# Performance work log

Measured on AMD Instinct MI355X. Metric: run time of the kernel, lower is better.

Reference implementation:

```python
import jax, jax.numpy as jnp
import numpy as np

SR = 22050
L = 2097153            # output_size = int(SR*95.109); equals NFFT//2+1 so spectral broadcast is well-defined
NFFT = 4194304         # 2**ceil(log2(L))
BANDS = [(1.0, 4.0), (4.0, 8.0), (8.0, 13.0), (13.0, 30.0), (30.0, 100.0), (100.0, 200.0)]
SPEC = [7.83, 528.0, 396.0, 2.5, 14.1, 432.0, 6.0, 30.0]
WIN = 15               # min(15, NFFT//100)
FREQS_NP = np.fft.rfftfreq(NFFT, 1.0 / SR).astype(np.float32)
FREQS = jnp.asarray(FREQS_NP)


def _freq_mod(sig, band_w, freq_w, harm_prog, tm_w1, tm_b1, tm_w2, tm_b2, tm_w3, tm_b3):
    t = jnp.arange(L, dtype=jnp.float32)
    Xf = jnp.fft.rfft(jnp.pad(sig, (0, NFFT - L)))            # [L] complex64
    # sequential band enhancements == product of per-band multipliers
    mult = jnp.ones((L,), jnp.float32)
    for b, (lo, hi) in enumerate(BANDS):
        c = (lo + hi) / 2.0
        w = (hi - lo) / 2.0
        mask = jnp.exp(-0.5 * ((FREQS - c) / (w / 2.0)) ** 2)
        mask = jnp.where((FREQS < lo) | (FREQS > hi), 0.0, mask)
        tmod = jnp.sin(2.0 * np.pi * c * t / SR)
        mult = mult * (1.0 + mask * band_w[b] * (1.0 + 0.2 * tmod))
    # harmonic progression (identical for every specific frequency -> compute once)
    tn = (t / L)[:, None]
    h = jax.nn.relu(tn @ tm_w1 + tm_b1)
    h = jax.nn.relu(h @ tm_w2 + tm_b2)
    mp = h @ tm_w3 + tm_b3                                    # [L, 8]
    chord_idx = jnp.floor(t / L * 8.0).astype(jnp.int32) % 8
    chord = harm_prog[chord_idx] * (1.0 + mp[:, 1] * jnp.sin(2.0 * np.pi * t / L))[:, None]
    prog_mean = chord.mean()
    # specific-frequency harmonic windows (static indices; commutative multiplies)
    smult = jnp.ones((L,), jnp.float32)
    for k, f in enumerate(SPEC):
        for m in (1.0, 2.0, 3.0, 4.0, 5.0):
            hf = f * m
            if hf >= SR / 2:
                continue
            hidx = int(np.argmin(np.abs(FREQS_NP - hf)))
            s = max(0, hidx - WIN)
            e = min(L - 1, hidx + WIN)
            win = jnp.asarray(np.exp(-0.5 * ((np.arange(s, e + 1) - hidx) / (WIN / 3.0)) ** 2).astype(np.float32))
            enh = freq_w[k] * win * (1.0 / m ** 1.2) * (1.0 + prog_mean)
            smult = smult.at[s:e + 1].multiply(1.0 + enh)
    Xf = Xf * mult * smult
    mag = jnp.abs(Xf)
    ph = jnp.angle(Xf)
    mag_s = jnp.concatenate([mag[:1], mag[1:-1] * 0.7 + mag[:-2] * 0.15 + mag[2:] * 0.15, mag[-1:]])
    Xc = mag_s * jnp.exp(1j * ph)
    return jnp.fft.irfft(Xc, n=NFFT)[:L]


def _conv1d(x, w, b, stride):
    y = jax.lax.conv_general_dilated(x, w, (stride,), [(2, 2)], dimension_numbers=("NCH", "OIH", "NCH"))
    return y + b[None, :, None]


def setup_inputs() -> dict:
    key = jax.random.key(0)
    ks = jax.random.split(key, 16)
    n = lambda k, s, sc=1.0: jax.random.normal(k, s, dtype=jnp.float32) * sc
    return {
        "z": n(ks[0], (1, 1, L)),
        "condition": n(ks[1], (1, 8)),
        "band_w": jnp.full((6,), 0.5, jnp.float32),
        "freq_w": jnp.full((8,), 0.3, jnp.float32),
        "harm_prog": n(ks[2], (8, 4)),
        "tm_w1": n(ks[3], (1, 32), 0.5), "tm_b1": jnp.zeros((32,), jnp.float32),
        "tm_w2": n(ks[4], (32, 16), 0.2), "tm_b2": jnp.zeros((16,), jnp.float32),
        "tm_w3": n(ks[5], (16, 8), 0.2), "tm_b3": jnp.zeros((8,), jnp.float32),
        "c1_w": n(ks[6], (32, 1, 5), 0.3), "c1_b": jnp.zeros((32,), jnp.float32),
        "c2_w": n(ks[7], (64, 32, 5), 0.08), "c2_b": jnp.zeros((64,), jnp.float32),
        "c3_w": n(ks[8], (128, 64, 5), 0.05), "c3_b": jnp.zeros((128,), jnp.float32),
        "mx_w1": n(ks[9], (192, 256), 0.07), "mx_b1": jnp.zeros((256,), jnp.float32),
        "mx_w2": n(ks[10], (256, 1), 0.06), "mx_b2": jnp.zeros((1,), jnp.float32),
    }


def reference(z, condition, band_w, freq_w, harm_prog, tm_w1, tm_b1, tm_w2, tm_b2, tm_w3, tm_b3,
              c1_w, c1_b, c2_w, c2_b, c3_w, c3_b, mx_w1, mx_b1, mx_w2, mx_b2):
    base = _freq_mod(z[0, 0], band_w, freq_w, harm_prog, tm_w1, tm_b1, tm_w2, tm_b2, tm_w3, tm_b3)[None, None, :]
    h = jax.nn.leaky_relu(_conv1d(base, c1_w, c1_b, 2), 0.2)
    h = jax.nn.leaky_relu(_conv1d(h, c2_w, c2_b, 2), 0.2)
    h = jax.nn.leaky_relu(_conv1d(h, c3_w, c3_b, 2), 0.2)
    feat = h.mean(axis=2)                                     # [1, 128]
    emb = jnp.zeros((1, 64), jnp.float32)                     # instrument_idx=None path
    mixed = jnp.concatenate([feat, emb], axis=1)              # [1, 192]
    out = jax.nn.leaky_relu(mixed @ mx_w1 + mx_b1, 0.2) @ mx_w2 + mx_b2
    return out
```

## Files before the change

kernel.cpp:

```cpp
#include <hip/hip_runtime.h>
#include <cmath>

#define LSIG  2097153
#define MH    2097152
#define NFFTC 4194304
#define NT    262144
#define NT64  32768
#define O1C   1048577
#define O2C   524289
#define O3C   262145

#define TO3   62
#define NB3   4229

#define A_OFF    0
#define B_OFF    16777216
#define PM_OFF   58720268
#define FEAT_OFF 58720272
#define W2Q_OFF  50331664
#define W3Q_OFF  50352144
#define W1Q_OFF  50434064

struct SmultTab { int hidx[40]; float inv12[40]; int fk[40]; int maxe; };

typedef short short8 __attribute__((ext_vector_type(8)));
typedef float f32x4v __attribute__((ext_vector_type(4)));

union AFrag { uint4 q; short8 s; };
union BFrag { uint4 q; unsigned int u[4]; short8 s; };

__device__ __forceinline__ float lrelu(float a){ return a > 0.0f ? a : 0.2f*a; }

__device__ __forceinline__ float hsin(float rev){ return __builtin_amdgcn_sinf(rev); }
__device__ __forceinline__ float hcos(float rev){ return __builtin_amdgcn_cosf(rev); }

__device__ __forceinline__ unsigned int rbf(float f) {
  unsigned int u = __float_as_uint(f);
  u += 0x7fffu + ((u >> 16) & 1u);
  return u >> 16;
}
__device__ __forceinline__ unsigned int pack_bf2(float a, float b) {
  return rbf(a) | (rbf(b) << 16);
}

__device__ __forceinline__ int swz1(int pos, int dw) {
  return (pos*16 + dw) ^ (((pos >> 1) & 7) << 2);
}
__device__ __forceinline__ int swz2(int pos, int dw) {
  return (pos*32 + dw) ^ (((pos >> 1) & 7) << 2);
}

__device__ __forceinline__ float2 cadd(float2 a, float2 b){ return make_float2(a.x+b.x, a.y+b.y); }
__device__ __forceinline__ float2 csub(float2 a, float2 b){ return make_float2(a.x-b.x, a.y-b.y); }
__device__ __forceinline__ float2 cmul(float2 a, float2 b){ return make_float2(a.x*b.x - a.y*b.y, a.x*b.y + a.y*b.x); }

template<bool FWD> __device__ __forceinline__ float2 jrot(float2 z){
  return FWD ? make_float2(z.y, -z.x) : make_float2(-z.y, z.x);
}

template<bool FWD> __device__ __forceinline__ void dft8(float2 v[8]) {
  const float cq = 0.70710678118654752440f;
  const float S  = FWD ? -1.0f : 1.0f;
  float2 e0 = cadd(v[0], v[4]), e1 = csub(v[0], v[4]);
  float2 e2 = cadd(v[2], v[6]), e3 = csub(v[2], v[6]);
  float2 E0 = cadd(e0, e2), E2 = csub(e0, e2);
  float2 jt = jrot<FWD>(e3);
  float2 E1 = cadd(e1, jt), E3 = csub(e1, jt);
  float2 o0 = cadd(v[1], v[5]), o1 = csub(v[1], v[5]);
  float2 o2 = cadd(v[3], v[7]), o3 = csub(v[3], v[7]);
  float2 O0 = cadd(o0, o2), O2 = csub(o0, o2);
  float2 jo = jrot<FWD>(o3);
  float2 O1 = cadd(o1, jo), O3 = csub(o1, jo);
  float2 T1 = make_float2(cq, S*cq), T3 = make_float2(-cq, S*cq);
  float2 w1 = cmul(T1, O1);
  float2 w2 = jrot<FWD>(O2);
  float2 w3 = cmul(T3, O3);
  v[0] = cadd(E0, O0); v[4] = csub(E0, O0);
  v[1] = cadd(E1, w1); v[5] = csub(E1, w1);
  v[2] = cadd(E2, w2); v[6] = csub(E2, w2);
  v[3] = cadd(E3, w3); v[7] = csub(E3, w3);
}

template<bool FWD>
__global__ __launch_bounds__(256) void kfft8(const float2* __restrict__ src,
                                             float2* __restrict__ dst, int Ns) {
  int j = blockIdx.x*256 + threadIdx.x;
  int m = j & (Ns - 1);
  const float ssg = FWD ? -1.0f : 1.0f;
  float frac = (float)m / (float)(Ns * 8);
  float2 v[8];
  v[0] = src[j];
#pragma unroll
  for (int r = 1; r < 8; ++r) {
    float2 a = src[j + r*NT];
    float rev = frac * (float)r;
    float sn = ssg * hsin(rev), cs = hcos(rev);
    v[r] = make_float2(a.x*cs - a.y*sn, a.x*sn + a.y*cs);
  }
  dft8<FWD>(v);
  int base = ((j - m) << 3) + m;
#pragma unroll
  for (int r = 0; r < 8; ++r) dst[base + r*Ns] = v[r];
}

template<bool FWD, bool FIRST>
__global__ __launch_bounds__(256) void kfft64(const float2* __restrict__ src,
                                              float2* __restrict__ dst, int Ns,
                                              const float* __restrict__ zin) {
  __shared__ float2 ex[32*65];
  const int t = threadIdx.x;
  const int b = t >> 3, i = t & 7;
  const int j = blockIdx.x*32 + b;
  const int m = j & (Ns - 1);
  const float ssg = FWD ? -1.0f : 1.0f;
  const float invden = 1.0f / (float)(64 * Ns);
  float2 v[8];
#pragma unroll
  for (int r1 = 0; r1 < 8; ++r1) {
    const int r = 8*r1 + i;
    const int n = j + r * NT64;
    float2 a;
    if (FIRST) {
      if (n < 1048576)       a = ((const float2*)zin)[n];
      else if (n == 1048576) a = make_float2(zin[2097152], 0.0f);
      else                   a = make_float2(0.0f, 0.0f);
    } else {
      a = src[n];
    }
    float rev = (float)(m * r) * invden;
    float sn = ssg * hsin(rev), cs = hcos(rev);
    v[r1] = make_float2(a.x*cs - a.y*sn, a.x*sn + a.y*cs);
  }
  dft8<FWD>(v);
#pragma unroll
  for (int k1 = 0; k1 < 8; ++k1) {
    float rev = (float)(i*k1) * 0.015625f;
    float sn = ssg * hsin(rev), cs = hcos(rev);
    ex[b*65 + k1*8 + i] = make_float2(v[k1].x*cs - v[k1].y*sn, v[k1].x*sn + v[k1].y*cs);
  }
  __syncthreads();
  float2 u[8];
#pragma unroll
  for (int r0 = 0; r0 < 8; ++r0) u[r0] = ex[b*65 + i*8 + r0];
  dft8<FWD>(u);
  const int base = (j - m)*64 + m;
#pragma unroll
  for (int k0 = 0; k0 < 8; ++k0) dst[base + (8*k0 + i)*Ns] = u[k0];
}

__global__ __launch_bounds__(256) void kprog(
    const float* __restrict__ tw1, const float* __restrict__ tb1,
    const float* __restrict__ tw2, const float* __restrict__ tb2,
    const float* __restrict__ tw3, const float* __restrict__ tb3,
    const float* __restrict__ hp, float* __restrict__ pm) {
  __shared__ float sw1[32], sb1[32], sw2[512], sb2[16], sw3[16], shp[8], sb31[1];
  __shared__ float red[256];
  const int tid = threadIdx.x;
  if (tid < 32) { sw1[tid] = tw1[tid]; sb1[tid] = tb1[tid]; }
  for (int q = tid; q < 512; q += 256) sw2[q] = tw2[q];
  if (tid < 16) { sb2[tid] = tb2[tid]; sw3[tid] = tw3[tid*8+1]; }
  if (tid < 8) { float s = 0.f; for (int j = 0; j < 4; ++j) s += hp[tid*4+j]; shp[tid] = s; }
  if (tid == 0) sb31[0] = tb3[1];
  __syncthreads();
  const int gid = blockIdx.x*256 + tid;
  const float Lf = 2097153.0f;
  float tnv[4], sv[4];
  int ci[4];
  float acc[4][16];
#pragma unroll
  for (int e = 0; e < 4; ++e) {
    float ti = (float)(gid + e*524288);
    float tn = ti / Lf;
    tnv[e] = tn;
    sv[e] = hsin(tn);
    ci[e] = ((int)floorf(tn * 8.0f)) & 7;
#pragma unroll
    for (int kk = 0; kk < 16; ++kk) acc[e][kk] = sb2[kk];
  }
  for (int j = 0; j < 32; ++j) {
    float a = sw1[j], b = sb1[j];
    float hj[4];
#pragma unroll
    for (int e = 0; e < 4; ++e) hj[e] = fmaxf(a*tnv[e] + b, 0.0f);
#pragma unroll
    for (int kk = 0; kk < 16; ++kk) {
      float w = sw2[j*16 + kk];
#pragma unroll
      for (int e = 0; e < 4; ++e) acc[e][kk] += hj[e]*w;
    }
  }
  float lsum = 0.0f;
#pragma unroll
  for (int e = 0; e < 4; ++e) {
    float mp1 = sb31[0];
#pragma unroll
    for (int kk = 0; kk < 16; ++kk) mp1 += fmaxf(acc[e][kk], 0.0f)*sw3[kk];
    lsum += shp[ci[e]] * (1.0f + mp1*sv[e]);
  }
  if (gid == 0) {
    float ti = 2097152.0f;
    float tn = ti / Lf;
    float a1[16];
    for (int kk = 0; kk < 16; ++kk) a1[kk] = sb2[kk];
    for (int j = 0; j < 32; ++j) {
      float h = fmaxf(sw1[j]*tn + sb1[j], 0.0f);
      for (int kk = 0; kk < 16; ++kk) a1[kk] += h*sw2[j*16+kk];
    }
    float mp1 = sb31[0];
    for (int kk = 0; kk < 16; ++kk) mp1 += fmaxf(a1[kk], 0.0f)*sw3[kk];
    float svx = hsin(tn);
    int cix = ((int)floorf(tn * 8.0f)) & 7;
    lsum += shp[cix] * (1.0f + mp1*svx);
  }
  red[tid] = lsum;
  __syncthreads();
  for (int off = 128; off > 0; off >>= 1) {
    if (tid < off) red[tid] += red[tid+off];
    __syncthreads();
  }
  if (tid == 0) atomicAdd(pm, red[0]);
}

__device__ __forceinline__ float2 xsplit(float2 zk, float2 zm, float rev) {
  float2 s  = make_float2(zk.x + zm.x, zk.y - zm.y);
  float2 dd = make_float2(zk.x - zm.x, zk.y + zm.y);
  float sn = -hsin(rev), cs = hcos(rev);
  float2 t1 = make_float2(cs*dd.x - sn*dd.y, cs*dd.y + sn*dd.x);
  return make_float2(0.5f*(s.x + t1.y), 0.5f*(s.y - t1.x));
}
__device__ __forceinline__ float2 scale_xc(float2 c, float mg, float ms) {
  if (mg > 0.0f) { float sc = ms/mg; return make_float2(c.x*sc, c.y*sc); }
  return make_float2(ms, 0.0f);
}
__device__ __forceinline__ float2 invpack(int n, float2 a, float2 b) {
  float2 s  = make_float2(a.x + b.x, a.y - b.y);
  float2 dd = make_float2(a.x - b.x, a.y + b.y);
  float rev = (float)n * (1.0f / (float)NFFTC);
  float sn = hsin(rev), cs = hcos(rev);
  float2 xo = make_float2(0.5f*(cs*dd.x - sn*dd.y), 0.5f*(cs*dd.y + sn*dd.x));
  const float sc = 1.0f / (float)MH;
  return make_float2((0.5f*s.x - xo.y)*sc, (0.5f*s.y + xo.x)*sc);
}

__global__ __launch_bounds__(256) void kspectral(const float2* __restrict__ Z,
    float2* __restrict__ A, const float* __restrict__ bwp,
    const float* __restrict__ fwp, const float* __restrict__ pm_in, SmultTab tab,
    const float* __restrict__ c1w, const float* __restrict__ c2w,
    const float* __restrict__ c3w, unsigned short* __restrict__ w1q,
    unsigned short* __restrict__ w2q, unsigned short* __restrict__ w3q) {
  const int bb = blockIdx.x;
  const int t = threadIdx.x;
  if (bb >= 4096) {
    int i = (bb - 4096)*256 + t;
    if (i < 1024) {
      int e = i & 7, quad = (i >> 3) & 3, ch = i >> 5;
      float v = (quad == 0 && e < 5) ? c1w[ch*5 + e] : 0.0f;
      w1q[i] = (unsigned short)rbf(v);
    }
    if (i < 10240) {
      int e = i & 7, quad = (i >> 3) & 3, kt = (i >> 5) % 5, ch = i / 160;
      int c1 = quad*8 + e;
      w2q[i] = (unsigned short)rbf(c2w[ch*160 + c1*5 + kt]);
    }
    if (i < 40960) {
      int e = i & 7, quad = (i >> 3) & 3, kt = (i >> 5) % 10, ch = i / 320;
      int c2 = (kt & 1)*32 + quad*8 + e;
      w3q[i] = (unsigned short)rbf(c3w[ch*320 + c2*5 + (kt >> 1)]);
    }
    return;
  }
  __shared__ float2 Xlo[258], Xhi[258];
  __shared__ float  Mlo[258], Mhi[258];
  const int k0 = bb * 256;
  const float pm1 = 1.0f + pm_in[0] * (1.0f/8388612.0f);
  for (int w = t; w < 258; w += 256) {
    int k = k0 - 1 + w;
    float2 zk = Z[k & (MH-1)];
    float2 zm = Z[(MH - k) & (MH-1)];
    {
      float2 X = xsplit(zk, zm, (float)k * (1.0f/(float)NFFTC));
      float mv = 1.0f;
      if (k <= 38050) {
        const float blo[6] = {1.0f,4.0f,8.0f,13.0f,30.0f,100.0f};
        const float bhi[6] = {4.0f,8.0f,13.0f,30.0f,100.0f,200.0f};
        const float bcn[6] = {2.5f,6.0f,10.5f,21.5f,65.0f,150.0f};
        const float bhw[6] = {0.75f,1.0f,1.25f,4.25f,17.5f,25.0f};
        float f = (float)((double)k * (22050.0/4194304.0));
#pragma unroll
        for (int b = 0; b < 6; ++b) {
          if (f >= blo[b] && f <= bhi[b]) {
            float q = (f - bcn[b]) / bhw[b];
            float mask = expf(-0.5f*q*q);
            double frd = (double)k * ((double)bcn[b] / 22050.0);
            frd -= floor(frd);
            float tm = hsin((float)frd);
            mv *= (1.0f + mask * bwp[b] * (1.0f + 0.2f*tm));
          }
        }
      }
      if (k <= tab.maxe) {
        for (int ww = 0; ww < 40; ++ww) {
          int dlt = k - tab.hidx[ww];
          if (dlt >= -15 && dlt <= 15) {
            float x = (float)dlt * 0.2f;
            float win = expf(-0.5f*x*x);
            float enh = fwp[tab.fk[ww]] * win * tab.inv12[ww] * pm1;
            mv *= (1.0f + enh);
          }
        }
      }
      X.x *= mv; X.y *= mv;
      Xlo[w] = X; Mlo[w] = sqrtf(X.x*X.x + X.y*X.y);
    }
    {
      float2 X = xsplit(zm, zk, (float)(MH - k) * (1.0f/(float)NFFTC));
      Xhi[w] = X; Mhi[w] = sqrtf(X.x*X.x + X.y*X.y);
    }
  }
  __syncthreads();
  const int k = k0 + t, w = t + 1;
  float msl = (k == 0) ? Mlo[w] : 0.7f*Mlo[w] + 0.15f*(Mlo[w-1] + Mlo[w+1]);
  float2 xl = scale_xc(Xlo[w], Mlo[w], msl);
  float msh = (k == 0) ? Mhi[w] : 0.7f*Mhi[w] + 0.15f*(Mhi[w+1] + Mhi[w-1]);
  float2 xh = scale_xc(Xhi[w], Mhi[w], msh);
  A[k] = invpack(k, xl, xh);
  if (k >= 1) A[MH - k] = invpack(MH - k, xh, xl);
  if (bb == 4095 && t == 255) {
    float2 Xm = Xlo[257]; float Mm = Mlo[257];
    float ms = 0.7f*Mm + 0.15f*(Mlo[256] + Mhi[256]);
    float2 xm = scale_xc(Xm, Mm, ms);
    A[1048576] = invpack(1048576, xm, xm);
  }
}

__global__ __launch_bounds__(256, 4) void kconv(const float* __restrict__ x,
    const unsigned short* __restrict__ w1q, const unsigned short* __restrict__ w2q,
    const unsigned short* __restrict__ w3q, const float* __restrict__ c1b,
    const float* __restrict__ c2b, const float* __restrict__ c3b,
    float* __restrict__ feat) {
  __shared__ float sb[552];
  __shared__ unsigned int sh1[4352];
  __shared__ unsigned int sh2[4224];
  __shared__ float sbias1[32], sbias2[64], sbias3[128];
  const int tid  = threadIdx.x;
  const int blk  = blockIdx.x;
  const int s3   = blk * TO3;
  const int lane = tid & 63;
  const int wv   = tid >> 6;
  const int col  = lane & 15;
  const int quad = lane >> 4;

  const uint4* W1 = (const uint4*)w1q;
  AFrag a1w[2];
#pragma unroll
  for (int mi = 0; mi < 2; ++mi)
    a1w[mi].q = W1[(mi*16 + col)*4 + quad];

  const uint4* W2 = (const uint4*)w2q;
  const int mt2 = (wv & 1) * 2;
  const int ntb2 = (wv >> 1) * 4;
  uint4 wk2[2][5];
#pragma unroll
  for (int mi = 0; mi < 2; ++mi)
#pragma unroll
    for (int kt = 0; kt < 5; ++kt)
      wk2[mi][kt] = W2[(((mt2+mi)*16 + col)*5 + kt)*4 + quad];

  {
    const int pb = 8*s3 - 14;
    for (int idx = tid; idx < 552; idx += 256) {
      int p = pb + idx;
      sb[idx] = (idx < 517 && p >= 0 && p < LSIG) ? x[p] : 0.0f;
    }
    if (tid < 64) sbias2[tid] = c2b[tid];
    else if (tid < 192) sbias3[tid-64] = c3b[tid-64];
    else if (tid < 224) sbias1[tid-192] = c1b[tid-192];
    if (tid < 128) sh2[4096 + tid] = 0u;
  }
  __syncthreads();

  {
    const int a1 = 4*s3 - 6;
    for (int nt = wv; nt < 17; nt += 4) {
      const int n = nt*16 + col;
      BFrag bf;
      if (quad == 0) {
        const float* ps = &sb[2*n];
        bf.u[0] = pack_bf2(ps[0], ps[1]);
        bf.u[1] = pack_bf2(ps[2], ps[3]);
        bf.u[2] = pack_bf2(ps[4], ps[5]);
        bf.u[3] = pack_bf2(ps[6], ps[7]);
      } else {
        bf.u[0] = 0u; bf.u[1] = 0u; bf.u[2] = 0u; bf.u[3] = 0u;
      }
      f32x4v acc[2];
      acc[0] = (f32x4v){0,0,0,0};
      acc[1] = (f32x4v){0,0,0,0};
      acc[0] = __builtin_amdgcn_mfma_f32_16x16x32_bf16(a1w[0].s, bf.s, acc[0], 0, 0, 0);
      acc[1] = __builtin_amdgcn_mfma_f32_16x16x32_bf16(a1w[1].s, bf.s, acc[1], 0, 0, 0);
      const int o1 = a1 + n;
      const bool ok = (n <= 257) && (o1 >= 0) && (o1 < O1C);
#pragma unroll
      for (int mi = 0; mi < 2; ++mi) {
        const int chb = mi*16 + quad*4;
        float v0 = ok ? lrelu(acc[mi][0] + sbias1[chb+0]) : 0.0f;
        float v1 = ok ? lrelu(acc[mi][1] + sbias1[chb+1]) : 0.0f;
        float v2 = ok ? lrelu(acc[mi][2] + sbias1[chb+2]) : 0.0f;
        float v3 = ok ? lrelu(acc[mi][3] + sbias1[chb+3]) : 0.0f;
        uint2 pk; pk.x = pack_bf2(v0, v1); pk.y = pack_bf2(v2, v3);
        *(uint2*)&sh1[swz1(n, mi*8 + quad*2)] = pk;
      }
    }
  }
  __syncthreads();

  f32x4v acc2[2][4];
#pragma unroll
  for (int mi = 0; mi < 2; ++mi)
#pragma unroll
    for (int nt = 0; nt < 4; ++nt) acc2[mi][nt] = (f32x4v){0,0,0,0};
#pragma unroll
  for (int kt = 0; kt < 5; ++kt) {
#pragma unroll
    for (int nt = 0; nt < 4; ++nt) {
      const int n = (ntb2 + nt)*16 + col;
      const int row = 2*n + kt;
      BFrag bf;
      bf.q = *(const uint4*)&sh1[swz1(row, quad*4)];
      AFrag a0, a1; a0.q = wk2[0][kt]; a1.q = wk2[1][kt];
      acc2[0][nt] = __builtin_amdgcn_mfma_f32_16x16x32_bf16(a0.s, bf.s, acc2[0][nt], 0, 0, 0);
      acc2[1][nt] = __builtin_amdgcn_mfma_f32_16x16x32_bf16(a1.s, bf.s, acc2[1][nt], 0, 0, 0);
    }
  }

  {
    const int a2 = 2*s3 - 2;
#pragma unroll
    for (int nt = 0; nt < 4; ++nt) {
      const int p = (ntb2 + nt)*16 + col;
      const int o2 = a2 + p;
      const bool ok = (o2 >= 0) && (o2 < O2C);
#pragma unroll
      for (int mi = 0; mi < 2; ++mi) {
        const int chb = (mt2+mi)*16 + quad*4;
        float v0 = ok ? lrelu(acc2[mi][nt][0] + sbias2[chb+0]) : 0.0f;
        float v1 = ok ? lrelu(acc2[mi][nt][1] + sbias2[chb+1]) : 0.0f;
        float v2 = ok ? lrelu(acc2[mi][nt][2] + sbias2[chb+2]) : 0.0f;
        float v3 = ok ? lrelu(acc2[mi][nt][3] + sbias2[chb+3]) : 0.0f;
        const int dwb = (mt2+mi)*8 + quad*2;
        uint2 pk; pk.x = pack_bf2(v0, v1); pk.y = pack_bf2(v2, v3);
        *(uint2*)&sh2[swz2(p, dwb)] = pk;
      }
    }
  }
  __syncthreads();

  {
    const uint4* W3 = (const uint4*)w3q;
    const int slot = (blk & 255) * 128;
#pragma unroll
    for (int pass = 0; pass < 2; ++pass) {
      const int mt = wv + 4*pass;
      uint4 wk3[10];
#pragma unroll
      for (int kt = 0; kt < 10; ++kt)
        wk3[kt] = W3[((mt*16 + col)*10 + kt)*4 + quad];
      f32x4v acc3[4];
#pragma unroll
      for (int nt = 0; nt < 4; ++nt) acc3[nt] = (f32x4v){0,0,0,0};
#pragma unroll
      for (int kt = 0; kt < 10; ++kt) {
        const int tap = kt >> 1;
        const int hh  = (kt & 1) * 16;
#pragma unroll
        for (int nt = 0; nt < 4; ++nt) {
          const int n = nt*16 + col;
          const int row = 2*n + tap;
          BFrag bf;
          bf.q = *(const uint4*)&sh2[swz2(row, hh + quad*4)];
          AFrag a; a.q = wk3[kt];
          acc3[nt] = __builtin_amdgcn_mfma_f32_16x16x32_bf16(a.s, bf.s, acc3[nt], 0, 0, 0);
        }
      }
#pragma unroll
      for (int r = 0; r < 4; ++r) {
        const int ch = mt*16 + quad*4 + r;
        const float bb = sbias3[ch];
        float v = 0.0f;
#pragma unroll
        for (int nt = 0; nt < 4; ++nt) {
          const int n = nt*16 + col;
          const bool ok = (n < TO3) && (s3 + n < O3C);
          if (ok) v += lrelu(acc3[nt][r] + bb);
        }
        v += __shfl_xor(v, 1);
        v += __shfl_xor(v, 2);
        v += __shfl_xor(v, 4);
        v += __shfl_xor(v, 8);
        if (col == 0) atomicAdd(&feat[slot + ch], v);
      }
    }
  }
}

__global__ __launch_bounds__(256) void kfinal(const float* __restrict__ feat,
    const float* __restrict__ mw1, const float* __restrict__ mb1,
    const float* __restrict__ mw2, const float* __restrict__ mb2,
    float* __restrict__ out) {
  __shared__ float sfeat[128];
  __shared__ float red[256];
  const int tid = threadIdx.x;
  if (tid < 128) {
    float s = 0.0f;
    for (int sl = 0; sl < 256; ++sl) s += feat[sl*128 + tid];
    sfeat[tid] = s / 262145.0f;
  }
  __syncthreads();
  float y = mb1[tid];
  for (int i = 0; i < 128; ++i) y += sfeat[i] * mw1[i*256 + tid];
  y = y > 0.0f ? y : 0.2f*y;
  red[tid] = y * mw2[tid];
  __syncthreads();
  for (int off = 128; off > 0; off >>= 1) {
    if (tid < off) red[tid] += red[tid+off];
    __syncthreads();
  }
  if (tid == 0) out[0] = red[0] + mb2[0];
}

extern "C" void kernel_launch(void* const* d_in, const int* in_sizes, int n_in,
                              void* d_out, int out_size, void* d_ws, size_t ws_size,
                              hipStream_t stream) {
  (void)in_sizes; (void)n_in; (void)out_size; (void)ws_size;
  const float* z   = (const float*)d_in[0];
  const float* bw  = (const float*)d_in[2];
  const float* fw  = (const float*)d_in[3];
  const float* hp  = (const float*)d_in[4];
  const float* tw1 = (const float*)d_in[5];
  const float* tb1 = (const float*)d_in[6];
  const float* tw2 = (const float*)d_in[7];
  const float* tb2 = (const float*)d_in[8];
  const float* tw3 = (const float*)d_in[9];
  const float* tb3 = (const float*)d_in[10];
  const float* c1w = (const float*)d_in[11];
  const float* c1b = (const float*)d_in[12];
  const float* c2w = (const float*)d_in[13];
  const float* c2b = (const float*)d_in[14];
  const float* c3w = (const float*)d_in[15];
  const float* c3b = (const float*)d_in[16];
  const float* mw1 = (const float*)d_in[17];
  const float* mb1 = (const float*)d_in[18];
  const float* mw2 = (const float*)d_in[19];
  const float* mb2 = (const float*)d_in[20];

  char* wsb = (char*)d_ws;
  float2* A    = (float2*)(wsb + A_OFF);
  float2* B    = (float2*)(wsb + B_OFF);
  float*  PM   = (float*)(wsb + PM_OFF);
  float*  FEAT = (float*)(wsb + FEAT_OFF);
  unsigned short* W1Q = (unsigned short*)(wsb + W1Q_OFF);
  unsigned short* W2Q = (unsigned short*)(wsb + W2Q_OFF);
  unsigned short* W3Q = (unsigned short*)(wsb + W3Q_OFF);

  SmultTab tab;
  {
    const double spec[8] = {7.83, 528.0, 396.0, 2.5, 14.1, 432.0, 6.0, 30.0};
    int n = 0, maxe = 0;
    for (int kk = 0; kk < 8; ++kk)
      for (int m = 1; m <= 5; ++m) {
        double hf = spec[kk] * (double)m;
        if (hf >= 11025.0) continue;
        int hidx = (int)std::floor(hf * (4194304.0/22050.0) + 0.5);
        tab.hidx[n]  = hidx;
        tab.inv12[n] = (float)(1.0/std::pow((double)m, 1.2));
        tab.fk[n]    = kk;
        if (hidx + 15 > maxe) maxe = hidx + 15;
        ++n;
      }
    tab.maxe = maxe;
  }

  (void)hipMemsetAsync(wsb + PM_OFF, 0, 4 + 131072, stream);
  kprog<<<2048,256,0,stream>>>(tw1,tb1,tw2,tb2,tw3,tb3,hp,PM);

  kfft64<true,true ><<<1024,256,0,stream>>>(A, A, 1,     z);
  kfft64<true,false><<<1024,256,0,stream>>>(A, B, 64,    z);
  kfft64<true,false><<<1024,256,0,stream>>>(B, A, 4096,  z);
  kfft8 <true>      <<<1024,256,0,stream>>>(A, B, 262144);

  kspectral<<<4256,256,0,stream>>>(B, A, bw, fw, PM, tab, c1w, c2w, c3w, W1Q, W2Q, W3Q);

  kfft64<false,false><<<1024,256,0,stream>>>(A, B, 1,     z);
  kfft64<false,false><<<1024,256,0,stream>>>(B, A, 64,    z);
  kfft64<false,false><<<1024,256,0,stream>>>(A, B, 4096,  z);
  kfft8 <false>      <<<1024,256,0,stream>>>(B, A, 262144);

  kconv<<<NB3,256,0,stream>>>((const float*)A, W1Q, W2Q, W3Q, c1b, c2b, c3b, FEAT);
  kfinal<<<1,256,0,stream>>>(FEAT, mw1, mb1, mw2, mb2, (float*)d_out);
}
```

Baseline: 316.5 us.

## Stage FFT64 passes through shared memory and fuse first pass with prog kernel

The radix-64 FFT kernel now loads a 64-column tile into skewed shared memory so global reads and writes are coalesced, and skips twiddles when Ns==1. The first forward pass is merged with the harmonic-progression reduction and the feature zeroing into one launch, which drops a separate kernel and most of the memset. Conv biases are folded into the MFMA accumulator initialisation instead of being read from shared memory, and bf16 packing uses the hardware pack instruction. The cost is extra shared memory and more syncthreads per FFT block, plus fewer, larger blocks.

```diff
diff --git a/kernel.cpp b/kernel.cpp
--- a/kernel.cpp
+++ b/kernel.cpp
@@ -40,7 +40,9 @@
   return u >> 16;
 }
 __device__ __forceinline__ unsigned int pack_bf2(float a, float b) {
-  return rbf(a) | (rbf(b) << 16);
+  unsigned int r;
+  asm("v_cvt_pk_bf16_f32 %0, %1, %2" : "=v"(r) : "v"(a), "v"(b));
+  return r;
 }
 
 __device__ __forceinline__ int swz1(int pos, int dw) {
@@ -103,66 +105,127 @@
   for (int r = 0; r < 8; ++r) dst[base + r*Ns] = v[r];
 }
 
-template<bool FWD, bool FIRST>
-__global__ __launch_bounds__(256) void kfft64(const float2* __restrict__ src,
-                                              float2* __restrict__ dst, int Ns,
-                                              const float* __restrict__ zin) {
-  __shared__ float2 ex[32*65];
+template<bool FWD>
+__global__ __launch_bounds__(512) void kfft64(const float2* __restrict__ src,
+                                              float2* __restrict__ dst, int Ns) {
+  __shared__ float2 stage[4096];
   const int t = threadIdx.x;
-  const int b = t >> 3, i = t & 7;
-  const int j = blockIdx.x*32 + b;
-  const int m = j & (Ns - 1);
+  const int jb = blockIdx.x * 64;
   const float ssg = FWD ? -1.0f : 1.0f;
   const float invden = 1.0f / (float)(64 * Ns);
+  for (int c = 0; c < 8; ++c) {
+    int idx = t + 512*c;
+    int jj = idx & 63, rr = idx >> 6;
+    stage[jj*64 + ((rr + 9*jj) & 63)] = src[jb + jj + rr*NT64];
+  }
+  __syncthreads();
+  const int bj = t >> 3, i = t & 7;
+  const int m = (jb + bj) & (Ns - 1);
   float2 v[8];
 #pragma unroll
   for (int r1 = 0; r1 < 8; ++r1) {
-    const int r = 8*r1 + i;
-    const int n = j + r * NT64;
-    float2 a;
-    if (FIRST) {
+    float2 a = stage[bj*64 + ((8*r1 + i + 9*bj) & 63)];
+    if (Ns > 1) {
+      const int r = 8*r1 + i;
+      float rev = (float)(m * r) * invden;
+      float sn = ssg * hsin(rev), cs = hcos(rev);
+      a = make_float2(a.x*cs - a.y*sn, a.x*sn + a.y*cs);
+    }
+    v[r1] = a;
+  }
+  dft8<FWD>(v);
+  __syncthreads();
+#pragma unroll
+  for (int k1 = 0; k1 < 8; ++k1) {
+    float rev = (float)(i*k1) * 0.015625f;
+    float sn = ssg * hsin(rev), cs = hcos(rev);
+    stage[bj*64 + ((k1*8 + i + 9*bj) & 63)] =
+      make_float2(v[k1].x*cs - v[k1].y*sn, v[k1].x*sn + v[k1].y*cs);
+  }
+  __syncthreads();
+  float2 u[8];
+#pragma unroll
+  for (int r0 = 0; r0 < 8; ++r0) u[r0] = stage[bj*64 + ((i*8 + r0 + 9*bj) & 63)];
+  dft8<FWD>(u);
+  __syncthreads();
+#pragma unroll
+  for (int k0 = 0; k0 < 8; ++k0)
+    stage[bj*64 + ((8*k0 + i + 9*bj) & 63)] = u[k0];
+  __syncthreads();
+  for (int c = 0; c < 8; ++c) {
+    int idx = t + 512*c;
+    int jj, k;
+    if (Ns == 1) { jj = idx >> 6; k = idx & 63; }
+    else         { jj = idx & 63; k = idx >> 6; }
+    int j2 = jb + jj, m2 = j2 & (Ns - 1);
+    dst[(j2 - m2)*64 + m2 + k*Ns] = stage[jj*64 + ((k + 9*jj) & 63)];
+  }
+}
+
+__global__ __launch_bounds__(512) void kfirst(
+    const float* __restrict__ zin, float2* __restrict__ dst,
+    const float* __restrict__ tw1, const float* __restrict__ tb1,
+    const float* __restrict__ tw2, const float* __restrict__ tb2,
+    const float* __restrict__ tw3, const float* __restrict__ tb3,
+    const float* __restrict__ hp, float* __restrict__ pm,
+    float* __restrict__ feat) {
+  __shared__ float2 stage[4096];
+  __shared__ float sw1[32], sb1[32], sw2[512], sb2[16], sw3[16], shp[8], sb31[1];
+  __shared__ float red[512];
+  const int t = threadIdx.x;
+  const int bb = blockIdx.x;
+  if (bb < 512) {
+    const int jb = bb * 64;
+    for (int c = 0; c < 8; ++c) {
+      int idx = t + 512*c;
+      int jj = idx & 63, rr = idx >> 6;
+      int n = jb + jj + rr*NT64;
+      float2 a;
       if (n < 1048576)       a = ((const float2*)zin)[n];
       else if (n == 1048576) a = make_float2(zin[2097152], 0.0f);
       else                   a = make_float2(0.0f, 0.0f);
-    } else {
-      a = src[n];
-    }
-    float rev = (float)(m * r) * invden;
-    float sn = ssg * hsin(rev), cs = hcos(rev);
-    v[r1] = make_float2(a.x*cs - a.y*sn, a.x*sn + a.y*cs);
-  }
-  dft8<FWD>(v);
-#pragma unroll
-  for (int k1 = 0; k1 < 8; ++k1) {
-    float rev = (float)(i*k1) * 0.015625f;
-    float sn = ssg * hsin(rev), cs = hcos(rev);
-    ex[b*65 + k1*8 + i] = make_float2(v[k1].x*cs - v[k1].y*sn, v[k1].x*sn + v[k1].y*cs);
-  }
-  __syncthreads();
-  float2 u[8];
-#pragma unroll
-  for (int r0 = 0; r0 < 8; ++r0) u[r0] = ex[b*65 + i*8 + r0];
-  dft8<FWD>(u);
-  const int base = (j - m)*64 + m;
-#pragma unroll
-  for (int k0 = 0; k0 < 8; ++k0) dst[base + (8*k0 + i)*Ns] = u[k0];
-}
-
-__global__ __launch_bounds__(256) void kprog(
-    const float* __restrict__ tw1, const float* __restrict__ tb1,
-    const float* __restrict__ tw2, const float* __restrict__ tb2,
-    const float* __restrict__ tw3, const float* __restrict__ tb3,
-    const float* __restrict__ hp, float* __restrict__ pm) {
-  __shared__ float sw1[32], sb1[32], sw2[512], sb2[16], sw3[16], shp[8], sb31[1];
-  __shared__ float red[256];
-  const int tid = threadIdx.x;
-  if (tid < 32) { sw1[tid] = tw1[tid]; sb1[tid] = tb1[tid]; }
-  for (int q = tid; q < 512; q += 256) sw2[q] = tw2[q];
-  if (tid < 16) { sb2[tid] = tb2[tid]; sw3[tid] = tw3[tid*8+1]; }
-  if (tid < 8) { float s = 0.f; for (int j = 0; j < 4; ++j) s += hp[tid*4+j]; shp[tid] = s; }
-  if (tid == 0) sb31[0] = tb3[1];
-  __syncthreads();
-  const int gid = blockIdx.x*256 + tid;
+      stage[jj*64 + ((rr + 9*jj) & 63)] = a;
+    }
+    __syncthreads();
+    const int bj = t >> 3, i = t & 7;
+    float2 v[8];
+#pragma unroll
+    for (int r1 = 0; r1 < 8; ++r1)
+      v[r1] = stage[bj*64 + ((8*r1 + i + 9*bj) & 63)];
+    dft8<true>(v);
+    __syncthreads();
+#pragma unroll
+    for (int k1 = 0; k1 < 8; ++k1) {
+      float rev = (float)(i*k1) * 0.015625f;
+      float sn = -hsin(rev), cs = hcos(rev);
+      stage[bj*64 + ((k1*8 + i + 9*bj) & 63)] =
+        make_float2(v[k1].x*cs - v[k1].y*sn, v[k1].x*sn + v[k1].y*cs);
+    }
+    __syncthreads();
+    float2 u[8];
+#pragma unroll
+    for (int r0 = 0; r0 < 8; ++r0) u[r0] = stage[bj*64 + ((i*8 + r0 + 9*bj) & 63)];
+    dft8<true>(u);
+    __syncthreads();
+#pragma unroll
+    for (int k0 = 0; k0 < 8; ++k0)
+      stage[bj*64 + ((8*k0 + i + 9*bj) & 63)] = u[k0];
+    __syncthreads();
+    for (int c = 0; c < 8; ++c) {
+      int idx = t + 512*c;
+      int jj = idx >> 6, k = idx & 63;
+      dst[(jb + jj)*64 + k] = stage[jj*64 + ((k + 9*jj) & 63)];
+    }
+    return;
+  }
+  if (t < 32) { sw1[t] = tw1[t]; sb1[t] = tb1[t]; }
+  sw2[t] = tw2[t];
+  if (t < 16) { sb2[t] = tb2[t]; sw3[t] = tw3[t*8+1]; }
+  if (t < 8) { float s = 0.f; for (int j = 0; j < 4; ++j) s += hp[t*4+j]; shp[t] = s; }
+  if (t == 0) sb31[0] = tb3[1];
+  __syncthreads();
+  const int gid = (bb - 512)*512 + t;
+  if (gid < 32768) feat[gid] = 0.0f;
   const float Lf = 2097153.0f;
   float tnv[4], sv[4];
   int ci[4];
@@ -212,13 +275,13 @@
     int cix = ((int)floorf(tn * 8.0f)) & 7;
     lsum += shp[cix] * (1.0f + mp1*svx);
   }
-  red[tid] = lsum;
-  __syncthreads();
-  for (int off = 128; off > 0; off >>= 1) {
-    if (tid < off) red[tid] += red[tid+off];
+  red[t] = lsum;
+  __syncthreads();
+  for (int off = 256; off > 0; off >>= 1) {
+    if (t < off) red[t] += red[t+off];
     __syncthreads();
   }
-  if (tid == 0) atomicAdd(pm, red[0]);
+  if (t == 0) atomicAdd(pm, red[0]);
 }
 
 __device__ __forceinline__ float2 xsplit(float2 zk, float2 zm, float rev) {
@@ -341,7 +404,6 @@
   __shared__ float sb[552];
   __shared__ unsigned int sh1[4352];
   __shared__ unsigned int sh2[4224];
-  __shared__ float sbias1[32], sbias2[64], sbias3[128];
   const int tid  = threadIdx.x;
   const int blk  = blockIdx.x;
   const int s3   = blk * TO3;
@@ -366,15 +428,21 @@
     for (int kt = 0; kt < 5; ++kt)
       wk2[mi][kt] = W2[(((mt2+mi)*16 + col)*5 + kt)*4 + quad];
 
+  float b1r[2][4], b2r[2][4];
+#pragma unroll
+  for (int mi = 0; mi < 2; ++mi)
+#pragma unroll
+    for (int r = 0; r < 4; ++r) {
+      b1r[mi][r] = c1b[mi*16 + quad*4 + r];
+      b2r[mi][r] = c2b[(mt2+mi)*16 + quad*4 + r];
+    }
+
   {
     const int pb = 8*s3 - 14;
     for (int idx = tid; idx < 552; idx += 256) {
       int p = pb + idx;
       sb[idx] = (idx < 517 && p >= 0 && p < LSIG) ? x[p] : 0.0f;
     }
-    if (tid < 64) sbias2[tid] = c2b[tid];
-    else if (tid < 192) sbias3[tid-64] = c3b[tid-64];
-    else if (tid < 224) sbias1[tid-192] = c1b[tid-192];
     if (tid < 128) sh2[4096 + tid] = 0u;
   }
   __syncthreads();
@@ -394,19 +462,18 @@
         bf.u[0] = 0u; bf.u[1] = 0u; bf.u[2] = 0u; bf.u[3] = 0u;
       }
       f32x4v acc[2];
-      acc[0] = (f32x4v){0,0,0,0};
-      acc[1] = (f32x4v){0,0,0,0};
+      acc[0] = (f32x4v){b1r[0][0], b1r[0][1], b1r[0][2], b1r[0][3]};
+      acc[1] = (f32x4v){b1r[1][0], b1r[1][1], b1r[1][2], b1r[1][3]};
       acc[0] = __builtin_amdgcn_mfma_f32_16x16x32_bf16(a1w[0].s, bf.s, acc[0], 0, 0, 0);
       acc[1] = __builtin_amdgcn_mfma_f32_16x16x32_bf16(a1w[1].s, bf.s, acc[1], 0, 0, 0);
       const int o1 = a1 + n;
       const bool ok = (n <= 257) && (o1 >= 0) && (o1 < O1C);
 #pragma unroll
       for (int mi = 0; mi < 2; ++mi) {
-        const int chb = mi*16 + quad*4;
-        float v0 = ok ? lrelu(acc[mi][0] + sbias1[chb+0]) : 0.0f;
-        float v1 = ok ? lrelu(acc[mi][1] + sbias1[chb+1]) : 0.0f;
-        float v2 = ok ? lrelu(acc[mi][2] + sbias1[chb+2]) : 0.0f;
-        float v3 = ok ? lrelu(acc[mi][3] + sbias1[chb+3]) : 0.0f;
+        float v0 = ok ? lrelu(acc[mi][0]) : 0.0f;
+        float v1 = ok ? lrelu(acc[mi][1]) : 0.0f;
+        float v2 = ok ? lrelu(acc[mi][2]) : 0.0f;
+        float v3 = ok ? lrelu(acc[mi][3]) : 0.0f;
         uint2 pk; pk.x = pack_bf2(v0, v1); pk.y = pack_bf2(v2, v3);
         *(uint2*)&sh1[swz1(n, mi*8 + quad*2)] = pk;
       }
@@ -418,7 +485,8 @@
 #pragma unroll
   for (int mi = 0; mi < 2; ++mi)
 #pragma unroll
-    for (int nt = 0; nt < 4; ++nt) acc2[mi][nt] = (f32x4v){0,0,0,0};
+    for (int nt = 0; nt < 4; ++nt)
+      acc2[mi][nt] = (f32x4v){b2r[mi][0], b2r[mi][1], b2r[mi][2], b2r[mi][3]};
 #pragma unroll
   for (int kt = 0; kt < 5; ++kt) {
 #pragma unroll
@@ -442,11 +510,10 @@
       const bool ok = (o2 >= 0) && (o2 < O2C);
 #pragma unroll
       for (int mi = 0; mi < 2; ++mi) {
-        const int chb = (mt2+mi)*16 + quad*4;
-        float v0 = ok ? lrelu(acc2[mi][nt][0] + sbias2[chb+0]) : 0.0f;
-        float v1 = ok ? lrelu(acc2[mi][nt][1] + sbias2[chb+1]) : 0.0f;
-        float v2 = ok ? lrelu(acc2[mi][nt][2] + sbias2[chb+2]) : 0.0f;
-        float v3 = ok ? lrelu(acc2[mi][nt][3] + sbias2[chb+3]) : 0.0f;
+        float v0 = ok ? lrelu(acc2[mi][nt][0]) : 0.0f;
+        float v1 = ok ? lrelu(acc2[mi][nt][1]) : 0.0f;
+        float v2 = ok ? lrelu(acc2[mi][nt][2]) : 0.0f;
+        float v3 = ok ? lrelu(acc2[mi][nt][3]) : 0.0f;
         const int dwb = (mt2+mi)*8 + quad*2;
         uint2 pk; pk.x = pack_bf2(v0, v1); pk.y = pack_bf2(v2, v3);
         *(uint2*)&sh2[swz2(p, dwb)] = pk;
@@ -465,9 +532,13 @@
 #pragma unroll
       for (int kt = 0; kt < 10; ++kt)
         wk3[kt] = W3[((mt*16 + col)*10 + kt)*4 + quad];
+      float b3r[4];
+#pragma unroll
+      for (int r = 0; r < 4; ++r) b3r[r] = c3b[mt*16 + quad*4 + r];
       f32x4v acc3[4];
 #pragma unroll
-      for (int nt = 0; nt < 4; ++nt) acc3[nt] = (f32x4v){0,0,0,0};
+      for (int nt = 0; nt < 4; ++nt)
+        acc3[nt] = (f32x4v){b3r[0], b3r[1], b3r[2], b3r[3]};
 #pragma unroll
       for (int kt = 0; kt < 10; ++kt) {
         const int tap = kt >> 1;
@@ -485,13 +556,12 @@
 #pragma unroll
       for (int r = 0; r < 4; ++r) {
         const int ch = mt*16 + quad*4 + r;
-        const float bb = sbias3[ch];
         float v = 0.0f;
 #pragma unroll
         for (int nt = 0; nt < 4; ++nt) {
           const int n = nt*16 + col;
           const bool ok = (n < TO3) && (s3 + n < O3C);
-          if (ok) v += lrelu(acc3[nt][r] + bb);
+          if (ok) v += lrelu(acc3[nt][r]);
         }
         v += __shfl_xor(v, 1);
         v += __shfl_xor(v, 2);
@@ -580,20 +650,20 @@
     tab.maxe = maxe;
   }
 
-  (void)hipMemsetAsync(wsb + PM_OFF, 0, 4 + 131072, stream);
-  kprog<<<2048,256,0,stream>>>(tw1,tb1,tw2,tb2,tw3,tb3,hp,PM);
-
-  kfft64<true,true ><<<1024,256,0,stream>>>(A, A, 1,     z);
-  kfft64<true,false><<<1024,256,0,stream>>>(A, B, 64,    z);
-  kfft64<true,false><<<1024,256,0,stream>>>(B, A, 4096,  z);
-  kfft8 <true>      <<<1024,256,0,stream>>>(A, B, 262144);
+  (void)hipMemsetAsync(wsb + PM_OFF, 0, 4, stream);
+
+  kfirst<<<1536,512,0,stream>>>(z, A, tw1,tb1,tw2,tb2,tw3,tb3,hp, PM, FEAT);
+
+  kfft64<true ><<<512,512,0,stream>>>(A, B, 64);
+  kfft64<true ><<<512,512,0,stream>>>(B, A, 4096);
+  kfft8 <true ><<<1024,256,0,stream>>>(A, B, 262144);
 
   kspectral<<<4256,256,0,stream>>>(B, A, bw, fw, PM, tab, c1w, c2w, c3w, W1Q, W2Q, W3Q);
 
-  kfft64<false,false><<<1024,256,0,stream>>>(A, B, 1,     z);
-  kfft64<false,false><<<1024,256,0,stream>>>(B, A, 64,    z);
-  kfft64<false,false><<<1024,256,0,stream>>>(A, B, 4096,  z);
-  kfft8 <false>      <<<1024,256,0,stream>>>(B, A, 262144);
+  kfft64<false><<<512,512,0,stream>>>(A, B, 1);
+  kfft64<false><<<512,512,0,stream>>>(B, A, 64);
+  kfft64<false><<<512,512,0,stream>>>(A, B, 4096);
+  kfft8 <false><<<1024,256,0,stream>>>(B, A, 262144);
 
   kconv<<<NB3,256,0,stream>>>((const float*)A, W1Q, W2Q, W3Q, c1b, c2b, c3b, FEAT);
   kfinal<<<1,256,0,stream>>>(FEAT, mw1, mb1, mw2, mb2, (float*)d_out);
```

Result: faster. 285.6 us (-9.8%).
